# Kernel tuning notes

Hardware: AMD Instinct MI355X
Metric: run time of the kernel (lower is better)

## Reference

```python
import jax, jax.numpy as jnp
import numpy as np

B, N, D, L, T = 64, 64, 6, 32, 2048
RHO = 0.7
W = np.float32(RHO ** (1.0 / L))  # per-step decay, rho ** (1/l_patts)


def setup_inputs() -> dict:
    key = jax.random.key(0)
    k1, k2 = jax.random.split(key)
    x = jax.random.normal(k1, (B, D, T), dtype=jnp.float32)
    patts = jax.random.normal(k2, (N, L), dtype=jnp.float32)  # torch.randn(n_patts, l_patts)
    w = jnp.float32(W)
    return {"x": x, "patts": patts, "w": w}


def _dtw_sq(x, patts, w):
    """Open-end (subsequence) weighted DTW of each pattern against each channel.

    DP recurrence (squared-distance cost, decay w on accumulated path):
      D[0, j] = c[0, j]                                    (free start in time)
      D[i, j] = c[i, j] + w * min(D[i-1, j], D[i, j-1], D[i-1, j-1])
    Output O[b, n, d, j] = D[L-1, j]  (distance of full pattern ending at time j).
    """
    b, d, t = x.shape
    n, l = patts.shape
    is_first = jnp.arange(l) == 0  # (L,)

    def col_step(Dprev_t, xt):
        # Dprev_t: (L, B, N, D) previous time column; xt: (B, D)
        # cost c[i] = (patts[n, i] - x[b, d, j])^2 -> (L, B, N, D)
        c_t = (patts.T[:, None, :, None] - xt[None, :, None, :]) ** 2
        Dprev_im1 = jnp.concatenate(
            [jnp.full_like(Dprev_t[:1], jnp.inf), Dprev_t[:-1]], axis=0)

        def cell(d_im1, inputs):
            ci, dp_i, dp_im1, first = inputs
            m = jnp.minimum(jnp.minimum(dp_i, dp_im1), d_im1)
            di = jnp.where(first, ci, ci + w * m)
            return di, di

        init = jnp.full(Dprev_t.shape[1:], jnp.inf, x.dtype)
        _, Dcol_t = jax.lax.scan(cell, init, (c_t, Dprev_t, Dprev_im1, is_first))
        return Dcol_t, Dcol_t[-1]  # carry full column, emit last row D[L-1, j]

    Dinit = jnp.full((l, b, n, d), jnp.inf, x.dtype)
    xs = jnp.moveaxis(x, -1, 0)  # (T, B, D)
    _, last = jax.lax.scan(col_step, Dinit, xs)  # (T, B, N, D)
    return jnp.moveaxis(last, 0, -1)  # (B, N, D, T)


def reference(x, patts, w):
    return jnp.sqrt(_dtw_sq(x, patts, w))
```

## Files before the change

### kernel.cpp

```cpp
#include <hip/hip_runtime.h>
#include <math.h>

#define TB 2048
#define LL 32
#define NP 64
#define DD 6
#define BB 64
#define NLANES 8
#define ROWS 4
#define CW 16
#define MSTEPS (TB/CW)


__global__ __launch_bounds__(256) void dtw_kernel(
    const float* __restrict__ x,
    const float* __restrict__ patts,
    const float* __restrict__ wptr,
    float* __restrict__ out)
{
    __shared__ float xs[TB];

    const int bid  = blockIdx.x;
    const int half = bid & 1;
    const int bd   = bid >> 1;
    const int tid  = threadIdx.x;

    const float4* xrow = (const float4*)(x + (size_t)bd * TB);
    float4* xs4 = (float4*)xs;
    xs4[tid]       = xrow[tid];
    xs4[tid + 256] = xrow[tid + 256];
    __syncthreads();

    const int g = tid >> 3;
    const int k = tid & 7;
    const int n = half * 32 + g;

    const float w = wptr[0];
    const float4 pv = *(const float4*)(patts + n * LL + k * ROWS);
    const float p0 = pv.x, p1 = pv.y, p2 = pv.z, p3 = pv.w;

    const int b = bd / DD, d = bd - (bd / DD) * DD;
    float* __restrict__ orow = out + (((size_t)b * NP + n) * DD + d) * TB;

    const bool k0 = (k == 0), k7 = (k == NLANES - 1);
    const float INF = __builtin_inff();

    float a0 = INF, a1 = INF, a2 = INF, a3 = INF;
    float diagC = INF;
    float r3[CW];
    #pragma unroll
    for (int c = 0; c < CW; ++c) r3[c] = INF;

    for (int m = 0; m < MSTEPS + NLANES - 1; ++m) {
        const int q = m - k;
        const bool valid = ((unsigned)q < (unsigned)MSTEPS);

        float recv[CW];
        #pragma unroll
        for (int c = 0; c < CW; ++c) recv[c] = __shfl_up(r3[c], 1, 64);

        const int qq = valid ? q : 0;
        const float4* xq = (const float4*)(xs + qq * CW);
        const float4 xA = xq[0], xB = xq[1], xC = xq[2], xD = xq[3];
        const float xv[CW] = {xA.x, xA.y, xA.z, xA.w,  xB.x, xB.y, xB.z, xB.w,
                              xC.x, xC.y, xC.z, xC.w,  xD.x, xD.y, xD.z, xD.w};

        float diag = diagC;
        #pragma unroll
        for (int c = 0; c < CW; ++c) {
            const float xvc = xv[c];
            float t0 = p0 - xvc, t1 = p1 - xvc, t2 = p2 - xvc, t3 = p3 - xvc;
            const float c0 = t0 * t0, c1 = t1 * t1, c2 = t2 * t2, c3 = t3 * t3;
            const float up = recv[c];
            const float l0 = a0, l1 = a1, l2 = a2, l3 = a3;

            const float m0 = fminf(fminf(l0, up), diag);
            const float v0 = k0 ? c0 : fmaf(w, m0, c0);
            const float m1 = fminf(fminf(l1, v0), l0);
            const float v1 = fmaf(w, m1, c1);
            const float m2 = fminf(fminf(l2, v1), l1);
            const float v2 = fmaf(w, m2, c2);
            const float m3 = fminf(fminf(l3, v2), l2);
            const float v3 = fmaf(w, m3, c3);

            a0 = v0; a1 = v1; a2 = v2; a3 = v3;
            diag = up;
            r3[c] = v3;
        }
        diagC = diag;

        if (k7 && valid) {
            float4* op = (float4*)(orow + q * CW);
            op[0] = make_float4(sqrtf(r3[0]),  sqrtf(r3[1]),  sqrtf(r3[2]),  sqrtf(r3[3]));
            op[1] = make_float4(sqrtf(r3[4]),  sqrtf(r3[5]),  sqrtf(r3[6]),  sqrtf(r3[7]));
            op[2] = make_float4(sqrtf(r3[8]),  sqrtf(r3[9]),  sqrtf(r3[10]), sqrtf(r3[11]));
            op[3] = make_float4(sqrtf(r3[12]), sqrtf(r3[13]), sqrtf(r3[14]), sqrtf(r3[15]));
        }
    }
}

extern "C" void kernel_launch(void* const* d_in, const int* in_sizes, int n_in,
                              void* d_out, int out_size, void* d_ws, size_t ws_size,
                              hipStream_t stream) {
    const float* x     = (const float*)d_in[0];
    const float* patts = (const float*)d_in[1];
    const float* wptr  = (const float*)d_in[2];
    float* out = (float*)d_out;

    dim3 grid(BB * DD * 2);
    dim3 block(256);
    dtw_kernel<<<grid, block, 0, stream>>>(x, patts, wptr, out);
}
```

Measured before the change: 304.6 us.

## Use DPP row shift for lane exchange, pad LDS and prefetch x chunks

Replaces the 16 per-step __shfl_up calls with a DPP row_shr:1 move. This removes the LDS-routed cross-lane permute traffic from the wavefront DP loop. The row-local shift is safe here because only lane k==0 sees a row boundary, and that lane ignores the received value. The x row is also stored in shared memory with a padded stride of 20 floats to cut bank conflicts. The next column chunk is now loaded one iteration ahead so LDS latency overlaps the DP arithmetic, at the cost of extra registers.

```diff
diff --git a/kernel.cpp b/kernel.cpp
--- a/kernel.cpp
+++ b/kernel.cpp
@@ -10,7 +10,14 @@
 #define ROWS 4
 #define CW 16
 #define MSTEPS (TB/CW)
+#define XSTRIDE 20
 
+
+__device__ __forceinline__ float dpp_shr1(float v) {
+    const int i = __float_as_int(v);
+    const int r = __builtin_amdgcn_update_dpp(i, i, 0x111, 0xF, 0xF, false);
+    return __int_as_float(r);
+}
 
 __global__ __launch_bounds__(256) void dtw_kernel(
     const float* __restrict__ x,
@@ -18,17 +25,22 @@
     const float* __restrict__ wptr,
     float* __restrict__ out)
 {
-    __shared__ float xs[TB];
+    __shared__ float xs[MSTEPS * XSTRIDE];
 
     const int bid  = blockIdx.x;
     const int half = bid & 1;
     const int bd   = bid >> 1;
     const int tid  = threadIdx.x;
 
+    const float INF = __builtin_inff();
+
     const float4* xrow = (const float4*)(x + (size_t)bd * TB);
-    float4* xs4 = (float4*)xs;
-    xs4[tid]       = xrow[tid];
-    xs4[tid + 256] = xrow[tid + 256];
+    #pragma unroll
+    for (int i = 0; i < 2; ++i) {
+        const int idx = tid + i * 256;
+        const int qb = idx >> 2, sub = idx & 3;
+        *(float4*)(xs + qb * XSTRIDE + sub * 4) = xrow[idx];
+    }
     __syncthreads();
 
     const int g = tid >> 3;
@@ -43,7 +55,6 @@
     float* __restrict__ orow = out + (((size_t)b * NP + n) * DD + d) * TB;
 
     const bool k0 = (k == 0), k7 = (k == NLANES - 1);
-    const float INF = __builtin_inff();
 
     float a0 = INF, a1 = INF, a2 = INF, a3 = INF;
     float diagC = INF;
@@ -51,17 +62,27 @@
     #pragma unroll
     for (int c = 0; c < CW; ++c) r3[c] = INF;
 
+    float4 xA = *(const float4*)(xs + 0);
+    float4 xB = *(const float4*)(xs + 4);
+    float4 xC = *(const float4*)(xs + 8);
+    float4 xD = *(const float4*)(xs + 12);
+
     for (int m = 0; m < MSTEPS + NLANES - 1; ++m) {
         const int q = m - k;
         const bool valid = ((unsigned)q < (unsigned)MSTEPS);
 
         float recv[CW];
         #pragma unroll
-        for (int c = 0; c < CW; ++c) recv[c] = __shfl_up(r3[c], 1, 64);
+        for (int c = 0; c < CW; ++c) recv[c] = dpp_shr1(r3[c]);
 
-        const int qq = valid ? q : 0;
-        const float4* xq = (const float4*)(xs + qq * CW);
-        const float4 xA = xq[0], xB = xq[1], xC = xq[2], xD = xq[3];
+        int qn = m + 1 - k;
+        qn = qn < 0 ? 0 : (qn > MSTEPS - 1 ? MSTEPS - 1 : qn);
+        const float* xbn = xs + qn * XSTRIDE;
+        const float4 nA = *(const float4*)(xbn + 0);
+        const float4 nB = *(const float4*)(xbn + 4);
+        const float4 nC = *(const float4*)(xbn + 8);
+        const float4 nD = *(const float4*)(xbn + 12);
+
         const float xv[CW] = {xA.x, xA.y, xA.z, xA.w,  xB.x, xB.y, xB.z, xB.w,
                               xC.x, xC.y, xC.z, xC.w,  xD.x, xD.y, xD.z, xD.w};
 
@@ -87,7 +108,7 @@
             diag = up;
             r3[c] = v3;
         }
-        diagC = diag;
+        diagC = recv[CW - 1];
 
         if (k7 && valid) {
             float4* op = (float4*)(orow + q * CW);
@@ -96,6 +117,8 @@
             op[2] = make_float4(sqrtf(r3[8]),  sqrtf(r3[9]),  sqrtf(r3[10]), sqrtf(r3[11]));
             op[3] = make_float4(sqrtf(r3[12]), sqrtf(r3[13]), sqrtf(r3[14]), sqrtf(r3[15]));
         }
+
+        xA = nA; xB = nB; xC = nC; xD = nD;
     }
 }
 
```

Measured after the change: 367.5 us. 1.21x slower.

## Use DPP row shifts for lane handoff and split into 64-thread blocks

Applied to the files above, without the earlier changes.

Each column's handoff to the next lane now uses a DPP row_shr:1 move folded into every DP step, replacing the batch of 16 __shfl_up calls that go through LDS permutes. The shift works within 16-lane rows. Lanes that would receive across a group boundary are k==0 lanes, which ignore the incoming value. Work is also split into 64-thread blocks covering 8 patterns each, giving eight times as many blocks with a 3-wave occupancy hint. The x buffer in shared memory gets a padded stride of 20 floats to reduce bank conflicts on the float4 reads.

```diff
diff --git a/kernel.cpp b/kernel.cpp
--- a/kernel.cpp
+++ b/kernel.cpp
@@ -6,95 +6,102 @@
 #define NP 64
 #define DD 6
 #define BB 64
-#define NLANES 8
-#define ROWS 4
 #define CW 16
 #define MSTEPS (TB/CW)
+#define XSTRIDE 20
 
 
-__global__ __launch_bounds__(256) void dtw_kernel(
+__device__ __forceinline__ float dpp_shr1(float v) {
+    const int i = __float_as_int(v);
+    const int r = __builtin_amdgcn_update_dpp(i, i, 0x111, 0xF, 0xF, false);
+    return __int_as_float(r);
+}
+
+#define STEP(XV, Y) {                                        \
+    const float up = dpp_shr1(Y);                            \
+    const float t0 = p0 - (XV);                              \
+    const float t1 = p1 - (XV);                              \
+    const float t2 = p2 - (XV);                              \
+    const float t3 = p3 - (XV);                              \
+    const float c0 = t0 * t0;                                \
+    const float m0 = fminf(fminf(a0, up), diag);             \
+    const float v0 = k0 ? c0 : fmaf(w, m0, c0);              \
+    const float m1 = fminf(fminf(a1, v0), a0);               \
+    const float v1 = fmaf(w, m1, t1 * t1);                   \
+    const float m2 = fminf(fminf(a2, v1), a1);               \
+    const float v2 = fmaf(w, m2, t2 * t2);                   \
+    const float m3 = fminf(fminf(a3, v2), a2);               \
+    const float v3 = fmaf(w, m3, t3 * t3);                   \
+    a0 = v0; a1 = v1; a2 = v2; a3 = v3;                      \
+    diag = up;                                               \
+    Y = v3;                                                  \
+}
+
+__global__ __launch_bounds__(64, 3) void dtw_kernel(
     const float* __restrict__ x,
     const float* __restrict__ patts,
     const float* __restrict__ wptr,
     float* __restrict__ out)
 {
-    __shared__ float xs[TB];
+    __shared__ float xs[MSTEPS * XSTRIDE];
 
-    const int bid  = blockIdx.x;
-    const int half = bid & 1;
-    const int bd   = bid >> 1;
-    const int tid  = threadIdx.x;
+    const int bid = blockIdx.x;
+    const int oct = bid & 7;
+    const int bd  = bid >> 3;
+    const int tid = threadIdx.x;
+
+    const float INF = __builtin_inff();
 
     const float4* xrow = (const float4*)(x + (size_t)bd * TB);
-    float4* xs4 = (float4*)xs;
-    xs4[tid]       = xrow[tid];
-    xs4[tid + 256] = xrow[tid + 256];
+    #pragma unroll
+    for (int i = 0; i < 8; ++i) {
+        const int idx = tid + i * 64;
+        *(float4*)(xs + (idx >> 2) * XSTRIDE + (idx & 3) * 4) = xrow[idx];
+    }
     __syncthreads();
 
     const int g = tid >> 3;
     const int k = tid & 7;
-    const int n = half * 32 + g;
+    const int n = oct * 8 + g;
 
     const float w = wptr[0];
-    const float4 pv = *(const float4*)(patts + n * LL + k * ROWS);
+    const float4 pv = *(const float4*)(patts + n * LL + k * 4);
     const float p0 = pv.x, p1 = pv.y, p2 = pv.z, p3 = pv.w;
 
     const int b = bd / DD, d = bd - (bd / DD) * DD;
     float* __restrict__ orow = out + (((size_t)b * NP + n) * DD + d) * TB;
 
-    const bool k0 = (k == 0), k7 = (k == NLANES - 1);
-    const float INF = __builtin_inff();
+    const bool k0 = (k == 0), k7 = (k == 7);
 
     float a0 = INF, a1 = INF, a2 = INF, a3 = INF;
-    float diagC = INF;
-    float r3[CW];
-    #pragma unroll
-    for (int c = 0; c < CW; ++c) r3[c] = INF;
+    float diag = INF;
+    float y0 = INF, y1 = INF, y2 = INF, y3 = INF,
+          y4 = INF, y5 = INF, y6 = INF, y7 = INF,
+          y8 = INF, y9 = INF, y10 = INF, y11 = INF,
+          y12 = INF, y13 = INF, y14 = INF, y15 = INF;
 
-    for (int m = 0; m < MSTEPS + NLANES - 1; ++m) {
+    for (int m = 0; m < MSTEPS + 7; ++m) {
         const int q = m - k;
         const bool valid = ((unsigned)q < (unsigned)MSTEPS);
+        const int qq = valid ? q : 0;
+        const float* xb = xs + qq * XSTRIDE;
 
-        float recv[CW];
-        #pragma unroll
-        for (int c = 0; c < CW; ++c) recv[c] = __shfl_up(r3[c], 1, 64);
+        const float4 xA = *(const float4*)(xb + 0);
+        const float4 xB = *(const float4*)(xb + 4);
+        const float4 xC = *(const float4*)(xb + 8);
+        const float4 xD = *(const float4*)(xb + 12);
 
-        const int qq = valid ? q : 0;
-        const float4* xq = (const float4*)(xs + qq * CW);
-        const float4 xA = xq[0], xB = xq[1], xC = xq[2], xD = xq[3];
-        const float xv[CW] = {xA.x, xA.y, xA.z, xA.w,  xB.x, xB.y, xB.z, xB.w,
-                              xC.x, xC.y, xC.z, xC.w,  xD.x, xD.y, xD.z, xD.w};
-
-        float diag = diagC;
-        #pragma unroll
-        for (int c = 0; c < CW; ++c) {
-            const float xvc = xv[c];
-            float t0 = p0 - xvc, t1 = p1 - xvc, t2 = p2 - xvc, t3 = p3 - xvc;
-            const float c0 = t0 * t0, c1 = t1 * t1, c2 = t2 * t2, c3 = t3 * t3;
-            const float up = recv[c];
-            const float l0 = a0, l1 = a1, l2 = a2, l3 = a3;
-
-            const float m0 = fminf(fminf(l0, up), diag);
-            const float v0 = k0 ? c0 : fmaf(w, m0, c0);
-            const float m1 = fminf(fminf(l1, v0), l0);
-            const float v1 = fmaf(w, m1, c1);
-            const float m2 = fminf(fminf(l2, v1), l1);
-            const float v2 = fmaf(w, m2, c2);
-            const float m3 = fminf(fminf(l3, v2), l2);
-            const float v3 = fmaf(w, m3, c3);
-
-            a0 = v0; a1 = v1; a2 = v2; a3 = v3;
-            diag = up;
-            r3[c] = v3;
-        }
-        diagC = diag;
+        STEP(xA.x, y0)  STEP(xA.y, y1)  STEP(xA.z, y2)  STEP(xA.w, y3)
+        STEP(xB.x, y4)  STEP(xB.y, y5)  STEP(xB.z, y6)  STEP(xB.w, y7)
+        STEP(xC.x, y8)  STEP(xC.y, y9)  STEP(xC.z, y10) STEP(xC.w, y11)
+        STEP(xD.x, y12) STEP(xD.y, y13) STEP(xD.z, y14) STEP(xD.w, y15)
 
         if (k7 && valid) {
             float4* op = (float4*)(orow + q * CW);
-            op[0] = make_float4(sqrtf(r3[0]),  sqrtf(r3[1]),  sqrtf(r3[2]),  sqrtf(r3[3]));
-            op[1] = make_float4(sqrtf(r3[4]),  sqrtf(r3[5]),  sqrtf(r3[6]),  sqrtf(r3[7]));
-            op[2] = make_float4(sqrtf(r3[8]),  sqrtf(r3[9]),  sqrtf(r3[10]), sqrtf(r3[11]));
-            op[3] = make_float4(sqrtf(r3[12]), sqrtf(r3[13]), sqrtf(r3[14]), sqrtf(r3[15]));
+            op[0] = make_float4(sqrtf(y0),  sqrtf(y1),  sqrtf(y2),  sqrtf(y3));
+            op[1] = make_float4(sqrtf(y4),  sqrtf(y5),  sqrtf(y6),  sqrtf(y7));
+            op[2] = make_float4(sqrtf(y8),  sqrtf(y9),  sqrtf(y10), sqrtf(y11));
+            op[3] = make_float4(sqrtf(y12), sqrtf(y13), sqrtf(y14), sqrtf(y15));
         }
     }
 }
@@ -107,7 +114,7 @@
     const float* wptr  = (const float*)d_in[2];
     float* out = (float*)d_out;
 
-    dim3 grid(BB * DD * 2);
-    dim3 block(256);
+    dim3 grid(BB * DD * 8);
+    dim3 block(64);
     dtw_kernel<<<grid, block, 0, stream>>>(x, patts, wptr, out);
 }
```

After: 364.8 us. 1.2x slower.
